# Kernel optimization log

Hardware: AMD Instinct MI355X
Metric: run time of the kernel (lower is better)

The kernel has to match this reference:

```python
import jax, jax.numpy as jnp
import numpy as np
from jax import lax

B, C, H, W = 8, 64, 128, 128
KS = 3          # kernel size
K = KS * KS     # kernel field = 9
PAD = 1


def conv2d(x, w, b):
    # x: [B,Cin,H,W], w: [Cout,Cin,kh,kw], 'same' 3x3 conv
    y = lax.conv_general_dilated(x, w, window_strides=(1, 1),
                                 padding=((PAD, PAD), (PAD, PAD)),
                                 dimension_numbers=('NCHW', 'OIHW', 'NCHW'))
    return y + b[None, :, None, None]


def modulated_deform_conv(x, offset, mask, weight, bias):
    # x:[B,C,H,W], offset:[B,2K,H,W] (dy,dx per tap), mask:[B,K,H,W]
    Bs, Cin, Hin, Win = x.shape
    off = offset.reshape(Bs, K, 2, Hin, Win)
    ky, kx = jnp.meshgrid(jnp.arange(KS), jnp.arange(KS), indexing='ij')
    ky = ky.reshape(K).astype(x.dtype)   # kernel tap row offsets 0..2
    kx = kx.reshape(K).astype(x.dtype)
    # sampling positions p = p0 + p_k + offset (stride=1, pad=1)
    py = (jnp.arange(Hin, dtype=x.dtype)[None, None, :, None] - PAD
          + ky[None, :, None, None] + off[:, :, 0])            # [B,K,H,W]
    px = (jnp.arange(Win, dtype=x.dtype)[None, None, None, :] - PAD
          + kx[None, :, None, None] + off[:, :, 1])            # [B,K,H,W]

    y0 = jnp.floor(py); x0 = jnp.floor(px)
    ly = py - y0; lx = px - x0                                  # frac parts
    y0i = y0.astype(jnp.int32); x0i = x0.astype(jnp.int32)

    x_flat = x.reshape(Bs, Cin, Hin * Win)

    def gather(iy, ix):
        valid = ((iy >= 0) & (iy < Hin) & (ix >= 0) & (ix < Win))
        flat = (jnp.clip(iy, 0, Hin - 1) * Win + jnp.clip(ix, 0, Win - 1))
        g = jax.vmap(lambda xb, ib: xb[:, ib])(x_flat, flat.reshape(Bs, -1))
        g = g.reshape(Bs, Cin, K, Hin, Win)
        return g * valid[:, None].astype(x.dtype)

    w00 = ((1 - ly) * (1 - lx))[:, None]  # [B,1,K,H,W]
    w01 = ((1 - ly) * lx)[:, None]
    w10 = (ly * (1 - lx))[:, None]
    w11 = (ly * lx)[:, None]

    val = (w00 * gather(y0i, x0i) + w01 * gather(y0i, x0i + 1)
           + w10 * gather(y0i + 1, x0i) + w11 * gather(y0i + 1, x0i + 1))
    val = val * mask[:, None]                                   # modulation
    out = jnp.einsum('ock,bckhw->bohw', weight.reshape(weight.shape[0], Cin, K), val)
    return out + bias[None, :, None, None]


def setup_inputs() -> dict:
    key = jax.random.key(0)
    ks = jax.random.split(key, 7)
    s = 0.05
    return {
        'x': jax.random.normal(ks[0], (B, C, H, W), jnp.float32),
        'w_om': jax.random.normal(ks[1], (3 * K, C, KS, KS), jnp.float32) * s,
        'b_om': jax.random.normal(ks[2], (3 * K,), jnp.float32) * s,
        'w_dc': jax.random.normal(ks[3], (C, C, KS, KS), jnp.float32) * s,
        'b_dc': jax.random.normal(ks[4], (C,), jnp.float32) * s,
        'w_c': jax.random.normal(ks[5], (C, C, KS, KS), jnp.float32) * s,
        'b_c': jax.random.normal(ks[6], (C,), jnp.float32) * s,
    }


def reference(x, w_om, b_om, w_dc, b_dc, w_c, b_c):
    om = conv2d(x, w_om, b_om)                       # [B,3K,H,W]
    offset, mask_raw = om[:, :2 * K], om[:, 2 * K:]
    mask = 2.0 * jax.nn.sigmoid(mask_raw)
    out = modulated_deform_conv(x, offset, mask, w_dc, b_dc)
    act = jnp.where(out > 0, out, 0.2 * out)         # LeakyReLU(0.2)
    return conv2d(act, w_c, b_c) + x
```

## Files before the change

kernel.cpp:

```cpp
#include <hip/hip_runtime.h>
#include <math.h>

#define Bn 8
#define Cn 64
#define Hn 128
#define Wn 128
#define HWn (Hn * Wn)

#define WOM_OFF 0
#define WDC_OFF 18432
#define WC_OFF 55296

typedef __attribute__((ext_vector_type(8))) short short8;
typedef __attribute__((ext_vector_type(4))) float floatx4;

__device__ __forceinline__ float bf2f(short s) {
  return __uint_as_float(((unsigned)(unsigned short)s) << 16);
}
__device__ __forceinline__ short f2bf(float f) {
  unsigned u = __float_as_uint(f);
  u += 0x7fff + ((u >> 16) & 1);
  return (short)(u >> 16);
}

__global__ __launch_bounds__(256) void k_prep_w(
    const float* __restrict__ w_om, const float* __restrict__ w_dc,
    const float* __restrict__ w_c, short* __restrict__ wt) {
  int idx = blockIdx.x * 256 + threadIdx.x;
  if (idx >= 92160) return;
  float v;
  if (idx < WDC_OFF) {
    int e = idx;
    int elem = e & 7, lane = (e >> 3) & 63, mt = (e >> 9) & 1, t = e >> 10;
    int kk = t % 9, cc = t / 9;
    int row = mt * 16 + (lane & 15);
    int cin = cc * 32 + (lane >> 4) * 8 + elem;
    v = (row < 27) ? w_om[(row * 64 + cin) * 9 + kk] : 0.f;
  } else {
    int e = (idx < WC_OFF) ? idx - WDC_OFF : idx - WC_OFF;
    const float* src = (idx < WC_OFF) ? w_dc : w_c;
    int elem = e & 7, lane = (e >> 3) & 63, mt = (e >> 9) & 3, t = e >> 11;
    int kk = t % 9, cc = t / 9;
    int row = mt * 16 + (lane & 15);
    int cin = cc * 32 + (lane >> 4) * 8 + elem;
    v = src[(row * 64 + cin) * 9 + kk];
  }
  wt[idx] = f2bf(v);
}

__global__ __launch_bounds__(256) void k_prep_x(const float* __restrict__ x,
                                                short* __restrict__ xT) {
  __shared__ float tile[64][129];
  const int bid = blockIdx.x;
  const int b = bid & 7, h = bid >> 3;
  const int tid = threadIdx.x;
  const float* xb = x + (size_t)b * 64 * HWn + h * Wn;
  for (int i = tid; i < 8192; i += 256) {
    int c = i >> 7, w = i & 127;
    tile[c][w] = xb[c * HWn + w];
  }
  __syncthreads();
  short* dst = xT + ((size_t)(b * Hn + h) * Wn) * 64;
  for (int i = tid; i < 2048; i += 256) {
    int w = i >> 4, c4 = (i & 15) * 4;
    short4 o;
    o.x = f2bf(tile[c4 + 0][w]);
    o.y = f2bf(tile[c4 + 1][w]);
    o.z = f2bf(tile[c4 + 2][w]);
    o.w = f2bf(tile[c4 + 3][w]);
    *(short4*)(dst + (size_t)w * 64 + c4) = o;
  }
}

__global__ __launch_bounds__(256, 5) void k_omdef(
    const short* __restrict__ xT, const short* __restrict__ wt,
    const float* __restrict__ b_om, const float* __restrict__ b_dc,
    short* __restrict__ actT) {
  __shared__ float som[27 * 66];
  __shared__ unsigned sbw[4 * 576];
  unsigned* sb01 = sbw;
  unsigned* sb23 = sbw + 576;
  unsigned* sw01 = sbw + 1152;
  unsigned* sw23 = sbw + 1728;

  const int bid = blockIdx.x;
  const int b = bid & 7;
  const int r = bid >> 3;
  const int h = r >> 1, w0 = (r & 1) * 64;
  const int tid = threadIdx.x;
  const int wave = tid >> 6, lane = tid & 63, quad = lane >> 4, lr = lane & 15;
  const short* xb = xT + (size_t)b * HWn * 64;
  const int pxl = wave * 16 + lr;
  const int gxp = w0 + pxl;

  floatx4 zf = {0.f, 0.f, 0.f, 0.f};

  floatx4 aco[2] = {zf, zf};
#pragma unroll 3
  for (int kk = 0; kk < 9; ++kk) {
    int ky = kk / 3, kx = kk - ky * 3;
    int gy = h + ky - 1, gx = gxp + kx - 1;
    bool ok = ((unsigned)gy < (unsigned)Hn) && ((unsigned)gx < (unsigned)Wn);
    int gyc = min(max(gy, 0), Hn - 1), gxc = min(max(gx, 0), Wn - 1);
    const short* rec = xb + (size_t)(gyc * Wn + gxc) * 64 + quad * 8;
#pragma unroll
    for (int cc = 0; cc < 2; ++cc) {
      short8 bf = *(const short8*)(rec + cc * 32);
      if (!ok) bf = (short8){0, 0, 0, 0, 0, 0, 0, 0};
      short8 a0 = *(const short8*)(wt + WOM_OFF +
                                   ((cc * 9 + kk) * 2 + 0) * 512 + lane * 8);
      short8 a1 = *(const short8*)(wt + WOM_OFF +
                                   ((cc * 9 + kk) * 2 + 1) * 512 + lane * 8);
      aco[0] = __builtin_amdgcn_mfma_f32_16x16x32_bf16(a0, bf, aco[0], 0, 0, 0);
      aco[1] = __builtin_amdgcn_mfma_f32_16x16x32_bf16(a1, bf, aco[1], 0, 0, 0);
    }
  }
#pragma unroll
  for (int mt = 0; mt < 2; ++mt) {
#pragma unroll
    for (int rr = 0; rr < 4; ++rr) {
      int co = mt * 16 + quad * 4 + rr;
      if (co < 27) {
        float v = aco[mt][rr] + b_om[co];
        if (co >= 18) v = 2.f / (1.f + expf(-v));
        som[co * 66 + pxl] = v;
      }
    }
  }
  __syncthreads();

  for (int pr = tid; pr < 576; pr += 256) {
    int k = pr >> 6, p = pr & 63;
    float offy = som[(2 * k) * 66 + p];
    float offx = som[(2 * k + 1) * 66 + p];
    float m = som[(18 + k) * 66 + p];
    float py = (float)(h - 1 + (k / 3)) + offy;
    float px_ = (float)(w0 + p - 1 + (k % 3)) + offx;
    float fy = floorf(py), fx = floorf(px_);
    float ly = py - fy, lx = px_ - fx;
    int iy0 = (int)fy, ix0 = (int)fx;
    int iy1 = iy0 + 1, ix1 = ix0 + 1;
    bool vy0 = (iy0 >= 0) && (iy0 < Hn);
    bool vy1 = (iy1 >= 0) && (iy1 < Hn);
    bool vx0 = (ix0 >= 0) && (ix0 < Wn);
    bool vx1 = (ix1 >= 0) && (ix1 < Wn);
    unsigned cy0 = (unsigned)min(max(iy0, 0), Hn - 1);
    unsigned cy1 = (unsigned)min(max(iy1, 0), Hn - 1);
    unsigned cx0 = (unsigned)min(max(ix0, 0), Wn - 1);
    unsigned cx1 = (unsigned)min(max(ix1, 0), Wn - 1);
    sb01[pr] = (cy0 * Wn + cx0) | ((cy0 * Wn + cx1) << 16);
    sb23[pr] = (cy1 * Wn + cx0) | ((cy1 * Wn + cx1) << 16);
    float u0 = (vy0 && vx0) ? (1.f - ly) * (1.f - lx) * m : 0.f;
    float u1 = (vy0 && vx1) ? (1.f - ly) * lx * m : 0.f;
    float u2 = (vy1 && vx0) ? ly * (1.f - lx) * m : 0.f;
    float u3 = (vy1 && vx1) ? ly * lx * m : 0.f;
    sw01[pr] = (unsigned)(unsigned short)f2bf(u0) |
               ((unsigned)(unsigned short)f2bf(u1) << 16);
    sw23[pr] = (unsigned)(unsigned short)f2bf(u2) |
               ((unsigned)(unsigned short)f2bf(u3) << 16);
  }
  __syncthreads();

  floatx4 acc[4] = {zf, zf, zf, zf};
#pragma unroll
  for (int cc = 0; cc < 2; ++cc) {
    const short* wbase = wt + WDC_OFF + cc * 18432;
#pragma unroll 3
    for (int kk = 0; kk < 9; ++kk) {
      int pr = kk * 64 + pxl;
      unsigned a01 = sb01[pr], a23 = sb23[pr];
      unsigned uw01 = sw01[pr], uw23 = sw23[pr];
      float u0 = bf2f((short)(uw01 & 0xFFFF));
      float u1 = bf2f((short)(uw01 >> 16));
      float u2 = bf2f((short)(uw23 & 0xFFFF));
      float u3 = bf2f((short)(uw23 >> 16));
      int co = cc * 32 + quad * 8;
      short8 q0 = *(const short8*)(xb + (size_t)(a01 & 0xFFFF) * 64 + co);
      short8 q1 = *(const short8*)(xb + (size_t)(a01 >> 16) * 64 + co);
      short8 q2 = *(const short8*)(xb + (size_t)(a23 & 0xFFFF) * 64 + co);
      short8 q3 = *(const short8*)(xb + (size_t)(a23 >> 16) * 64 + co);
      short8 bf;
#pragma unroll
      for (int e = 0; e < 8; ++e) {
        float f = u0 * bf2f(q0[e]) + u1 * bf2f(q1[e]) + u2 * bf2f(q2[e]) +
                  u3 * bf2f(q3[e]);
        bf[e] = f2bf(f);
      }
#pragma unroll
      for (int mt = 0; mt < 4; ++mt) {
        short8 am = *(const short8*)(wbase + (kk * 4 + mt) * 512 + lane * 8);
        acc[mt] = __builtin_amdgcn_mfma_f32_16x16x32_bf16(am, bf, acc[mt], 0, 0, 0);
      }
    }
  }

  short* ab = actT + ((size_t)(b * Hn + h) * Wn + w0) * 64;
#pragma unroll
  for (int mt = 0; mt < 4; ++mt) {
    int c0 = mt * 16 + quad * 4;
    short4 o;
    float v;
    v = acc[mt][0] + b_dc[c0 + 0]; o.x = f2bf(v > 0.f ? v : 0.2f * v);
    v = acc[mt][1] + b_dc[c0 + 1]; o.y = f2bf(v > 0.f ? v : 0.2f * v);
    v = acc[mt][2] + b_dc[c0 + 2]; o.z = f2bf(v > 0.f ? v : 0.2f * v);
    v = acc[mt][3] + b_dc[c0 + 3]; o.w = f2bf(v > 0.f ? v : 0.2f * v);
    *(short4*)(ab + (size_t)pxl * 64 + c0) = o;
  }
}

__global__ __launch_bounds__(256, 5) void k_conv_out(
    const short* __restrict__ actT, const short* __restrict__ wt,
    const float* __restrict__ b_c, const float* __restrict__ x,
    float* __restrict__ out) {
  __shared__ __attribute__((aligned(16))) float ot[64 * 66];

  const int bid = blockIdx.x;
  const int b = bid & 7;
  const int r = bid >> 3;
  const int h = r >> 1, w0 = (r & 1) * 64;
  const int tid = threadIdx.x;
  const int wave = tid >> 6, lane = tid & 63, quad = lane >> 4, lr = lane & 15;
  const short* ab = actT + (size_t)b * HWn * 64;
  const int pxl = wave * 16 + lr;
  const int gxp = w0 + pxl;

  floatx4 zf = {0.f, 0.f, 0.f, 0.f};
  floatx4 acc[4] = {zf, zf, zf, zf};

#pragma unroll
  for (int cc = 0; cc < 2; ++cc) {
    const short* wbase = wt + WC_OFF + cc * 18432;
#pragma unroll 3
    for (int kk = 0; kk < 9; ++kk) {
      int ky = kk / 3, kx = kk - ky * 3;
      int gy = h + ky - 1, gx = gxp + kx - 1;
      bool ok = ((unsigned)gy < (unsigned)Hn) && ((unsigned)gx < (unsigned)Wn);
      int gyc = min(max(gy, 0), Hn - 1), gxc = min(max(gx, 0), Wn - 1);
      short8 bf = *(const short8*)(ab + (size_t)(gyc * Wn + gxc) * 64 +
                                   cc * 32 + quad * 8);
      if (!ok) bf = (short8){0, 0, 0, 0, 0, 0, 0, 0};
#pragma unroll
      for (int mt = 0; mt < 4; ++mt) {
        short8 am = *(const short8*)(wbase + (kk * 4 + mt) * 512 + lane * 8);
        acc[mt] = __builtin_amdgcn_mfma_f32_16x16x32_bf16(am, bf, acc[mt], 0, 0, 0);
      }
    }
  }

#pragma unroll
  for (int mt = 0; mt < 4; ++mt) {
#pragma unroll
    for (int rr = 0; rr < 4; ++rr) {
      ot[(mt * 16 + quad * 4 + rr) * 66 + pxl] = acc[mt][rr];
    }
  }
  __syncthreads();

  const int row = tid >> 2, seg = tid & 3;
  const float bias = b_c[row];
  const size_t gbase = ((size_t)(b * 64 + row) * Hn + h) * Wn + w0 + seg * 16;
  const float* xr = x + gbase;
  float* op = out + gbase;
#pragma unroll
  for (int j = 0; j < 4; ++j) {
    floatx4 t = *(const floatx4*)&ot[row * 66 + seg * 16 + j * 4];
    floatx4 xv = *(const floatx4*)&xr[j * 4];
    t = t + xv;
    t[0] += bias; t[1] += bias; t[2] += bias; t[3] += bias;
    *(floatx4*)&op[j * 4] = t;
  }
}

extern "C" void kernel_launch(void* const* d_in, const int* in_sizes, int n_in,
                              void* d_out, int out_size, void* d_ws,
                              size_t ws_size, hipStream_t stream) {
  const float* x = (const float*)d_in[0];
  const float* w_om = (const float*)d_in[1];
  const float* b_om = (const float*)d_in[2];
  const float* w_dc = (const float*)d_in[3];
  const float* b_dc = (const float*)d_in[4];
  const float* w_c = (const float*)d_in[5];
  const float* b_c = (const float*)d_in[6];
  float* out = (float*)d_out;

  short* xT = (short*)d_ws;
  short* actT = xT + (size_t)Bn * HWn * 64;
  short* wt = actT + (size_t)Bn * HWn * 64;

  k_prep_w<<<dim3(360), 256, 0, stream>>>(w_om, w_dc, w_c, wt);
  k_prep_x<<<dim3(1024), 256, 0, stream>>>(x, xT);
  k_omdef<<<dim3(2048), 256, 0, stream>>>(xT, wt, b_om, b_dc, actT);
  k_conv_out<<<dim3(2048), 256, 0, stream>>>(actT, wt, b_c, x, out);
}
```

Baseline: 256.3 us.

## Use full-row 512-thread blocks, inline deform sampling, stage conv rows in LDS

Both main kernels now process a whole 128-pixel image row per 512-thread block instead of half rows. In the offset/deform kernel, the per-tap sampling coordinates and bilinear weights are computed directly in registers by each lane. This replaces staging them through shared memory and drops two block barriers in favour of a wave-local LDS wait. The output conv first loads three activation rows into swizzled shared memory and reads its 3x3 taps from there, cutting repeated global loads. The cost is redundant per-quad sampling math, higher per-block register and LDS pressure, and fewer, larger blocks.

Result: faster. 235.4 us (-8.1%).

```diff
diff --git a/kernel.cpp b/kernel.cpp
--- a/kernel.cpp
+++ b/kernel.cpp
@@ -72,41 +72,35 @@
   }
 }
 
-__global__ __launch_bounds__(256, 5) void k_omdef(
+__global__ __launch_bounds__(512, 4) void k_omdef(
     const short* __restrict__ xT, const short* __restrict__ wt,
     const float* __restrict__ b_om, const float* __restrict__ b_dc,
     short* __restrict__ actT) {
-  __shared__ float som[27 * 66];
-  __shared__ unsigned sbw[4 * 576];
-  unsigned* sb01 = sbw;
-  unsigned* sb23 = sbw + 576;
-  unsigned* sw01 = sbw + 1152;
-  unsigned* sw23 = sbw + 1728;
+  __shared__ float som[27 * 132];
 
   const int bid = blockIdx.x;
   const int b = bid & 7;
-  const int r = bid >> 3;
-  const int h = r >> 1, w0 = (r & 1) * 64;
+  const int h = bid >> 3;
   const int tid = threadIdx.x;
   const int wave = tid >> 6, lane = tid & 63, quad = lane >> 4, lr = lane & 15;
   const short* xb = xT + (size_t)b * HWn * 64;
   const int pxl = wave * 16 + lr;
-  const int gxp = w0 + pxl;
 
   floatx4 zf = {0.f, 0.f, 0.f, 0.f};
+  const short8 zz = (short8){0, 0, 0, 0, 0, 0, 0, 0};
 
   floatx4 aco[2] = {zf, zf};
 #pragma unroll 3
   for (int kk = 0; kk < 9; ++kk) {
     int ky = kk / 3, kx = kk - ky * 3;
-    int gy = h + ky - 1, gx = gxp + kx - 1;
+    int gy = h + ky - 1, gx = pxl + kx - 1;
     bool ok = ((unsigned)gy < (unsigned)Hn) && ((unsigned)gx < (unsigned)Wn);
     int gyc = min(max(gy, 0), Hn - 1), gxc = min(max(gx, 0), Wn - 1);
     const short* rec = xb + (size_t)(gyc * Wn + gxc) * 64 + quad * 8;
 #pragma unroll
     for (int cc = 0; cc < 2; ++cc) {
       short8 bf = *(const short8*)(rec + cc * 32);
-      if (!ok) bf = (short8){0, 0, 0, 0, 0, 0, 0, 0};
+      if (!ok) bf = zz;
       short8 a0 = *(const short8*)(wt + WOM_OFF +
                                    ((cc * 9 + kk) * 2 + 0) * 512 + lane * 8);
       short8 a1 = *(const short8*)(wt + WOM_OFF +
@@ -123,78 +117,79 @@
       if (co < 27) {
         float v = aco[mt][rr] + b_om[co];
         if (co >= 18) v = 2.f / (1.f + expf(-v));
-        som[co * 66 + pxl] = v;
+        som[co * 132 + pxl] = v;
       }
     }
   }
-  __syncthreads();
-
-  for (int pr = tid; pr < 576; pr += 256) {
-    int k = pr >> 6, p = pr & 63;
-    float offy = som[(2 * k) * 66 + p];
-    float offx = som[(2 * k + 1) * 66 + p];
-    float m = som[(18 + k) * 66 + p];
-    float py = (float)(h - 1 + (k / 3)) + offy;
-    float px_ = (float)(w0 + p - 1 + (k % 3)) + offx;
+  asm volatile("s_waitcnt lgkmcnt(0)" ::: "memory");
+
+  floatx4 acc[4] = {zf, zf, zf, zf};
+  const short* wdc = wt + WDC_OFF;
+  const int cq = quad * 8;
+#pragma unroll 3
+  for (int kk = 0; kk < 9; ++kk) {
+    float offy = som[(2 * kk) * 132 + pxl];
+    float offx = som[(2 * kk + 1) * 132 + pxl];
+    float m = som[(18 + kk) * 132 + pxl];
+    float py = (float)(h - 1 + (kk / 3)) + offy;
+    float px_ = (float)(pxl - 1 + (kk % 3)) + offx;
     float fy = floorf(py), fx = floorf(px_);
     float ly = py - fy, lx = px_ - fx;
     int iy0 = (int)fy, ix0 = (int)fx;
     int iy1 = iy0 + 1, ix1 = ix0 + 1;
-    bool vy0 = (iy0 >= 0) && (iy0 < Hn);
-    bool vy1 = (iy1 >= 0) && (iy1 < Hn);
-    bool vx0 = (ix0 >= 0) && (ix0 < Wn);
-    bool vx1 = (ix1 >= 0) && (ix1 < Wn);
+    bool vy0 = ((unsigned)iy0 < (unsigned)Hn);
+    bool vy1 = ((unsigned)iy1 < (unsigned)Hn);
+    bool vx0 = ((unsigned)ix0 < (unsigned)Wn);
+    bool vx1 = ((unsigned)ix1 < (unsigned)Wn);
     unsigned cy0 = (unsigned)min(max(iy0, 0), Hn - 1);
     unsigned cy1 = (unsigned)min(max(iy1, 0), Hn - 1);
     unsigned cx0 = (unsigned)min(max(ix0, 0), Wn - 1);
     unsigned cx1 = (unsigned)min(max(ix1, 0), Wn - 1);
-    sb01[pr] = (cy0 * Wn + cx0) | ((cy0 * Wn + cx1) << 16);
-    sb23[pr] = (cy1 * Wn + cx0) | ((cy1 * Wn + cx1) << 16);
+    unsigned d0 = cy0 * Wn + cx0, d1 = cy0 * Wn + cx1;
+    unsigned d2 = cy1 * Wn + cx0, d3 = cy1 * Wn + cx1;
     float u0 = (vy0 && vx0) ? (1.f - ly) * (1.f - lx) * m : 0.f;
     float u1 = (vy0 && vx1) ? (1.f - ly) * lx * m : 0.f;
     float u2 = (vy1 && vx0) ? ly * (1.f - lx) * m : 0.f;
     float u3 = (vy1 && vx1) ? ly * lx * m : 0.f;
-    sw01[pr] = (unsigned)(unsigned short)f2bf(u0) |
-               ((unsigned)(unsigned short)f2bf(u1) << 16);
-    sw23[pr] = (unsigned)(unsigned short)f2bf(u2) |
-               ((unsigned)(unsigned short)f2bf(u3) << 16);
-  }
-  __syncthreads();
-
-  floatx4 acc[4] = {zf, zf, zf, zf};
-#pragma unroll
-  for (int cc = 0; cc < 2; ++cc) {
-    const short* wbase = wt + WDC_OFF + cc * 18432;
-#pragma unroll 3
-    for (int kk = 0; kk < 9; ++kk) {
-      int pr = kk * 64 + pxl;
-      unsigned a01 = sb01[pr], a23 = sb23[pr];
-      unsigned uw01 = sw01[pr], uw23 = sw23[pr];
-      float u0 = bf2f((short)(uw01 & 0xFFFF));
-      float u1 = bf2f((short)(uw01 >> 16));
-      float u2 = bf2f((short)(uw23 & 0xFFFF));
-      float u3 = bf2f((short)(uw23 >> 16));
-      int co = cc * 32 + quad * 8;
-      short8 q0 = *(const short8*)(xb + (size_t)(a01 & 0xFFFF) * 64 + co);
-      short8 q1 = *(const short8*)(xb + (size_t)(a01 >> 16) * 64 + co);
-      short8 q2 = *(const short8*)(xb + (size_t)(a23 & 0xFFFF) * 64 + co);
-      short8 q3 = *(const short8*)(xb + (size_t)(a23 >> 16) * 64 + co);
-      short8 bf;
-#pragma unroll
-      for (int e = 0; e < 8; ++e) {
-        float f = u0 * bf2f(q0[e]) + u1 * bf2f(q1[e]) + u2 * bf2f(q2[e]) +
-                  u3 * bf2f(q3[e]);
-        bf[e] = f2bf(f);
-      }
-#pragma unroll
-      for (int mt = 0; mt < 4; ++mt) {
-        short8 am = *(const short8*)(wbase + (kk * 4 + mt) * 512 + lane * 8);
-        acc[mt] = __builtin_amdgcn_mfma_f32_16x16x32_bf16(am, bf, acc[mt], 0, 0, 0);
-      }
-    }
-  }
-
-  short* ab = actT + ((size_t)(b * Hn + h) * Wn + w0) * 64;
+
+    short8 q0 = *(const short8*)(xb + (size_t)d0 * 64 + cq);
+    short8 q1 = *(const short8*)(xb + (size_t)d1 * 64 + cq);
+    short8 q2 = *(const short8*)(xb + (size_t)d2 * 64 + cq);
+    short8 q3 = *(const short8*)(xb + (size_t)d3 * 64 + cq);
+    short8 r0 = *(const short8*)(xb + (size_t)d0 * 64 + 32 + cq);
+    short8 r1 = *(const short8*)(xb + (size_t)d1 * 64 + 32 + cq);
+    short8 r2 = *(const short8*)(xb + (size_t)d2 * 64 + 32 + cq);
+    short8 r3 = *(const short8*)(xb + (size_t)d3 * 64 + 32 + cq);
+
+    short8 bf0, bf1;
+#pragma unroll
+    for (int e = 0; e < 8; ++e) {
+      float f = u0 * bf2f(q0[e]) + u1 * bf2f(q1[e]) + u2 * bf2f(q2[e]) +
+                u3 * bf2f(q3[e]);
+      bf0[e] = f2bf(f);
+    }
+#pragma unroll
+    for (int e = 0; e < 8; ++e) {
+      float f = u0 * bf2f(r0[e]) + u1 * bf2f(r1[e]) + u2 * bf2f(r2[e]) +
+                u3 * bf2f(r3[e]);
+      bf1[e] = f2bf(f);
+    }
+
+#pragma unroll
+    for (int mt = 0; mt < 4; ++mt) {
+      short8 a0 = *(const short8*)(wdc + ((0 * 9 + kk) * 4 + mt) * 512 +
+                                   lane * 8);
+      acc[mt] = __builtin_amdgcn_mfma_f32_16x16x32_bf16(a0, bf0, acc[mt], 0, 0, 0);
+    }
+#pragma unroll
+    for (int mt = 0; mt < 4; ++mt) {
+      short8 a1 = *(const short8*)(wdc + ((1 * 9 + kk) * 4 + mt) * 512 +
+                                   lane * 8);
+      acc[mt] = __builtin_amdgcn_mfma_f32_16x16x32_bf16(a1, bf1, acc[mt], 0, 0, 0);
+    }
+  }
+
+  short* ab = actT + ((size_t)(b * Hn + h) * Wn) * 64;
 #pragma unroll
   for (int mt = 0; mt < 4; ++mt) {
     int c0 = mt * 16 + quad * 4;
@@ -208,62 +203,75 @@
   }
 }
 
-__global__ __launch_bounds__(256, 5) void k_conv_out(
+__global__ __launch_bounds__(512, 4) void k_conv_out(
     const short* __restrict__ actT, const short* __restrict__ wt,
     const float* __restrict__ b_c, const float* __restrict__ x,
     float* __restrict__ out) {
-  __shared__ __attribute__((aligned(16))) float ot[64 * 66];
+  __shared__ __attribute__((aligned(16))) short rows[24576];
 
   const int bid = blockIdx.x;
   const int b = bid & 7;
-  const int r = bid >> 3;
-  const int h = r >> 1, w0 = (r & 1) * 64;
+  const int h = bid >> 3;
   const int tid = threadIdx.x;
   const int wave = tid >> 6, lane = tid & 63, quad = lane >> 4, lr = lane & 15;
   const short* ab = actT + (size_t)b * HWn * 64;
   const int pxl = wave * 16 + lr;
-  const int gxp = w0 + pxl;
 
   floatx4 zf = {0.f, 0.f, 0.f, 0.f};
+  const short8 zz = (short8){0, 0, 0, 0, 0, 0, 0, 0};
   floatx4 acc[4] = {zf, zf, zf, zf};
+  short8* rows8 = (short8*)rows;
+
+  {
+    const short8* ar8 = (const short8*)ab;
+    for (int i = tid; i < 3072; i += 512) {
+      int rr = i >> 10, c = i & 1023;
+      int px = c >> 3, sl = c & 7;
+      int gy = min(max(h - 1 + rr, 0), Hn - 1);
+      short8 v = ar8[(size_t)(gy * Wn + px) * 8 + sl];
+      rows8[(rr << 10) + (px << 3) + (sl ^ (px & 7))] = v;
+    }
+  }
+  __syncthreads();
 
 #pragma unroll
   for (int cc = 0; cc < 2; ++cc) {
-    const short* wbase = wt + WC_OFF + cc * 18432;
-#pragma unroll 3
+#pragma unroll
     for (int kk = 0; kk < 9; ++kk) {
       int ky = kk / 3, kx = kk - ky * 3;
-      int gy = h + ky - 1, gx = gxp + kx - 1;
-      bool ok = ((unsigned)gy < (unsigned)Hn) && ((unsigned)gx < (unsigned)Wn);
-      int gyc = min(max(gy, 0), Hn - 1), gxc = min(max(gx, 0), Wn - 1);
-      short8 bf = *(const short8*)(ab + (size_t)(gyc * Wn + gxc) * 64 +
-                                   cc * 32 + quad * 8);
-      if (!ok) bf = (short8){0, 0, 0, 0, 0, 0, 0, 0};
+      int gy = h + ky - 1, gxx = pxl + kx - 1;
+      bool ok = ((unsigned)gy < (unsigned)Hn) && ((unsigned)gxx < (unsigned)Wn);
+      int gxc = min(max(gxx, 0), Wn - 1);
+      short8 bf = rows8[(ky << 10) + (gxc << 3) + ((cc * 4 + quad) ^ (gxc & 7))];
+      if (!ok) bf = zz;
 #pragma unroll
       for (int mt = 0; mt < 4; ++mt) {
-        short8 am = *(const short8*)(wbase + (kk * 4 + mt) * 512 + lane * 8);
+        short8 am = *(const short8*)(wt + WC_OFF + cc * 18432 +
+                                     (kk * 4 + mt) * 512 + lane * 8);
         acc[mt] = __builtin_amdgcn_mfma_f32_16x16x32_bf16(am, bf, acc[mt], 0, 0, 0);
       }
     }
   }
-
+  __syncthreads();
+
+  float* ot = (float*)rows;
 #pragma unroll
   for (int mt = 0; mt < 4; ++mt) {
 #pragma unroll
     for (int rr = 0; rr < 4; ++rr) {
-      ot[(mt * 16 + quad * 4 + rr) * 66 + pxl] = acc[mt][rr];
+      ot[(mt * 16 + quad * 4 + rr) * 132 + pxl] = acc[mt][rr];
     }
   }
   __syncthreads();
 
-  const int row = tid >> 2, seg = tid & 3;
+  const int row = tid >> 3, seg = tid & 7;
   const float bias = b_c[row];
-  const size_t gbase = ((size_t)(b * 64 + row) * Hn + h) * Wn + w0 + seg * 16;
+  const size_t gbase = ((size_t)(b * 64 + row) * Hn + h) * Wn + seg * 16;
   const float* xr = x + gbase;
   float* op = out + gbase;
 #pragma unroll
   for (int j = 0; j < 4; ++j) {
-    floatx4 t = *(const floatx4*)&ot[row * 66 + seg * 16 + j * 4];
+    floatx4 t = *(const floatx4*)&ot[row * 132 + seg * 16 + j * 4];
     floatx4 xv = *(const floatx4*)&xr[j * 4];
     t = t + xv;
     t[0] += bias; t[1] += bias; t[2] += bias; t[3] += bias;
@@ -289,6 +297,6 @@
 
   k_prep_w<<<dim3(360), 256, 0, stream>>>(w_om, w_dc, w_c, wt);
   k_prep_x<<<dim3(1024), 256, 0, stream>>>(x, xT);
-  k_omdef<<<dim3(2048), 256, 0, stream>>>(xT, wt, b_om, b_dc, actT);
-  k_conv_out<<<dim3(2048), 256, 0, stream>>>(actT, wt, b_c, x, out);
-}
+  k_omdef<<<dim3(1024), 512, 0, stream>>>(xT, wt, b_om, b_dc, actT);
+  k_conv_out<<<dim3(1024), 512, 0, stream>>>(actT, wt, b_c, x, out);
+}
```
